# Kernel tuning notes

Hardware: AMD Instinct MI355X
Metric: run time of the kernel (lower is better)

Reference implementation:

```python
import jax, jax.numpy as jnp
import numpy as np

NB = 4
QN = -(2 ** (NB - 1))   # -8
QP = 2 ** (NB - 1) - 1  # 7
EPS = 1e-5


def _grad_scale(x, g):
    # forward: x, backward: grad * g (LSQ gradient scaling)
    return x * g + jax.lax.stop_gradient(x - x * g)


def _round_pass(x):
    # round with straight-through estimator
    return x + jax.lax.stop_gradient(jnp.round(x) - x)


def _lsq(v, alpha, qn, qp):
    # LSQ fake quantize-dequantize with learnable step size alpha
    g = 1.0 / np.sqrt(v.size * qp)
    a = _grad_scale(alpha, g)
    return _round_pass(jnp.clip(v / a, qn, qp)) * a


def _bn(x, g, b, m, v):
    # eval-mode BatchNorm2d over channel dim of NCHW
    s = (g * jax.lax.rsqrt(v + EPS))[None, :, None, None]
    return (x - m[None, :, None, None]) * s + b[None, :, None, None]


def _conv(x, w, stride, pad, groups):
    return jax.lax.conv_general_dilated(
        x, w, (stride, stride), pad,
        dimension_numbers=('NCHW', 'OIHW', 'NCHW'),
        feature_group_count=groups)


def setup_inputs() -> dict:
    key = jax.random.key(0)
    ks = jax.random.split(key, 4)
    inp, oup, hid = 96, 96, 576
    B, H, W = 32, 28, 28
    d = {}
    d['x'] = jax.random.normal(ks[0], (B, inp, H, W), jnp.float32)
    d['w1'] = jax.random.normal(ks[1], (hid, inp, 1, 1), jnp.float32) * 0.1
    d['w2'] = jax.random.normal(ks[2], (hid, 1, 3, 3), jnp.float32) * 0.1
    d['w3'] = jax.random.normal(ks[3], (oup, hid, 1, 1), jnp.float32) * 0.1
    for i, c in zip((1, 2, 3), (hid, hid, oup)):
        d[f'aw{i}'] = jnp.full((1,), 0.05, jnp.float32)  # weight step size
        d[f'ax{i}'] = jnp.full((1,), 0.5, jnp.float32)   # activation step size
        d[f'g{i}'] = jnp.ones((c,), jnp.float32)
        d[f'b{i}'] = jnp.zeros((c,), jnp.float32)
        d[f'm{i}'] = jnp.zeros((c,), jnp.float32)
        d[f'v{i}'] = jnp.ones((c,), jnp.float32)
    return d


def reference(x, w1, w2, w3, aw1, ax1, g1, b1, m1, v1,
              aw2, ax2, g2, b2, m2, v2, aw3, ax3, g3, b3, m3, v3):
    hid = w1.shape[0]
    # 1x1 expand conv (LSQ on activation and weight)
    h = _conv(_lsq(x, ax1, QN, QP), _lsq(w1, aw1, QN, QP), 1, [(0, 0), (0, 0)], 1)
    h = jnp.clip(_bn(h, g1, b1, m1, v1), 0.0, 6.0)
    # 3x3 depthwise conv, stride 1
    h = _conv(_lsq(h, ax2, QN, QP), _lsq(w2, aw2, QN, QP), 1, [(1, 1), (1, 1)], hid)
    h = jnp.clip(_bn(h, g2, b2, m2, v2), 0.0, 6.0)
    # 1x1 project conv
    h = _conv(_lsq(h, ax3, QN, QP), _lsq(w3, aw3, QN, QP), 1, [(0, 0), (0, 0)], 1)
    h = _bn(h, g3, b3, m3, v3)
    # identity residual (stride==1 and inp==oup)
    return x + h
```

## Files before the change

### kernel.cpp

```cpp
#include <hip/hip_runtime.h>

#define EPSF 1e-5f

typedef int      int4v   __attribute__((ext_vector_type(4)));
typedef int      int2v   __attribute__((ext_vector_type(2)));
typedef float    float4v __attribute__((ext_vector_type(4)));
typedef _Float16 half8   __attribute__((ext_vector_type(8)));
typedef _Float16 half4   __attribute__((ext_vector_type(4)));

#define QH1H_OFF 0
#define QH2T_OFF 28901376
#define W1P_OFF  43352064
#define W3P_OFF  (W1P_OFF + 55296)
#define W2H_OFF  (W3P_OFF + 55296)
#define S1B1_OFF (W2H_OFF + 10368)
#define S2B2_OFF (S1B1_OFF + 4608)
#define S3B3_OFF (S2B2_OFF + 4608)

__device__ __forceinline__ float lsq_q(float v, float a) {
    float t = v / a;
    t = fminf(fmaxf(t, -8.0f), 7.0f);
    return rintf(t);
}

__device__ __forceinline__ long q8pack_w(const float* s, float a) {
    unsigned long long v = 0;
    #pragma unroll
    for (int j = 0; j < 8; ++j) {
        int q = (int)lsq_q(s[j], a);
        v |= (unsigned long long)(q & 255) << (8 * j);
    }
    return (long)v;
}

__global__ __launch_bounds__(256)
void prep_w(const float* __restrict__ w1, const float* __restrict__ w2,
            const float* __restrict__ w3,
            const float* aw1, const float* ax1, const float* ax2,
            const float* aw2, const float* ax3, const float* aw3,
            const float* __restrict__ g1, const float* __restrict__ b1,
            const float* __restrict__ m1, const float* __restrict__ v1,
            const float* __restrict__ g2, const float* __restrict__ b2,
            const float* __restrict__ m2, const float* __restrict__ v2,
            const float* __restrict__ g3, const float* __restrict__ b3,
            const float* __restrict__ m3, const float* __restrict__ v3,
            long* __restrict__ w1p, long* __restrict__ w3p,
            _Float16* __restrict__ w2h,
            float* __restrict__ s1b1, float* __restrict__ s2b2,
            float* __restrict__ s3b3) {
    int id = blockIdx.x * 256 + threadIdx.x;
    if (id < 6912) {
        int l = id & 63, t = id >> 6;
        int kc = t % 3, ct = t / 3;
        int co = ct * 16 + (l & 15);
        int ci0 = kc * 32 + (l >> 4) * 8;
        w1p[id] = q8pack_w(w1 + co * 96 + ci0, aw1[0]);
    } else if (id < 13824) {
        int i = id - 6912;
        int l = i & 63, t = i >> 6;
        int kc = t % 18, ct = t / 18;
        int co = ct * 16 + (l & 15);
        int ci0 = kc * 32 + (l >> 4) * 8;
        w3p[i] = q8pack_w(w3 + co * 576 + ci0, aw3[0]);
    } else if (id < 19008) {
        int i = id - 13824;
        int c = i % 576, tap = i / 576;
        w2h[i] = (_Float16)lsq_q(w2[c * 9 + tap], aw2[0]);
    } else if (id < 19584) {
        int c = id - 19008;
        float s = g1[c] / sqrtf(v1[c] + EPSF);
        float A = aw1[0] * ax1[0];
        float inv = 1.0f / ax2[0];
        s1b1[c] = A * s * inv;
        s1b1[576 + c] = (b1[c] - m1[c] * s) * inv;
    } else if (id < 20160) {
        int c = id - 19584;
        float s = g2[c] / sqrtf(v2[c] + EPSF);
        float A = ax2[0] * aw2[0];
        float inv = 1.0f / ax3[0];
        s2b2[c] = A * s * inv;
        s2b2[576 + c] = (b2[c] - m2[c] * s) * inv;
    } else if (id < 20256) {
        int c = id - 20160;
        float s = g3[c] / sqrtf(v3[c] + EPSF);
        float A = ax3[0] * aw3[0];
        s3b3[c] = A * s;
        s3b3[96 + c] = b3[c] - m3[c] * s;
    }
}

__global__ __launch_bounds__(256)
void conv1_mfma(const float* __restrict__ x, const long* __restrict__ w1p,
                const float* ax1, const float* __restrict__ s1b1,
                _Float16* __restrict__ qh1h) {
    const int tid = threadIdx.x;
    const int w = tid >> 6, l = tid & 63;
    const int quad = l >> 4, c16 = l & 15;
    const int n0 = blockIdx.x * 64, cs = blockIdx.y;
    const int n = n0 + w * 16 + c16;
    const int bi = n / 784, p = n - bi * 784;
    const float inv1 = 1.0f / ax1[0];

    long bfr[3];
    #pragma unroll
    for (int kc = 0; kc < 3; ++kc) {
        const float* xs = x + (bi * 96 + kc * 32 + quad * 8) * 784 + p;
        unsigned long long v = 0;
        #pragma unroll
        for (int j = 0; j < 8; ++j) {
            float t = xs[j * 784] * inv1;
            t = fminf(fmaxf(t, -8.0f), 7.0f);
            int q = (int)rintf(t);
            v |= (unsigned long long)(q & 255) << (8 * j);
        }
        bfr[kc] = (long)v;
    }

    int4v acc[12];
    #pragma unroll
    for (int i = 0; i < 12; ++i) { acc[i][0] = 0; acc[i][1] = 0; acc[i][2] = 0; acc[i][3] = 0; }

    #pragma unroll
    for (int kc = 0; kc < 3; ++kc)
        #pragma unroll
        for (int ct = 0; ct < 12; ++ct)
            acc[ct] = __builtin_amdgcn_mfma_i32_16x16x32_i8(
                w1p[((cs * 12 + ct) * 3 + kc) * 64 + l], bfr[kc], acc[ct], 0, 0, 0);

    _Float16* orow = qh1h + n * 576;
    #pragma unroll
    for (int ct = 0; ct < 12; ++ct) {
        int co0 = cs * 192 + ct * 16 + quad * 4;
        float4v S = *(const float4v*)(s1b1 + co0);
        float4v B = *(const float4v*)(s1b1 + 576 + co0);
        half4 h;
        #pragma unroll
        for (int r = 0; r < 4; ++r) {
            float t = fmaf((float)acc[ct][r], S[r], B[r]);
            t = fminf(fmaxf(t, 0.0f), 7.0f);
            h[r] = (_Float16)rintf(t);
        }
        *(half4*)(orow + co0) = h;
    }
}

__global__ __launch_bounds__(256)
void dw_k(const _Float16* __restrict__ qh1h, const _Float16* __restrict__ w2h,
          const float* __restrict__ s2b2, signed char* __restrict__ qh2T) {
    int idx = blockIdx.x * 256 + threadIdx.x;
    int n = idx / 72, g = idx - (idx / 72) * 72;
    int c0 = g * 8;
    int p = n % 784;
    int hh = p / 28, ww = p - hh * 28;
    const _Float16* base = qh1h + n * 576 + c0;

    half8 acc;
    #pragma unroll
    for (int j = 0; j < 8; ++j) acc[j] = (_Float16)0.0f;

    #pragma unroll
    for (int t = 0; t < 9; ++t) {
        const int dh = t / 3 - 1, dc = t % 3 - 1;
        int ih = hh + dh, iw = ww + dc;
        if (ih >= 0 && ih < 28 && iw >= 0 && iw < 28) {
            half8 xv = *(const half8*)(base + (dh * 28 + dc) * 576);
            half8 wv = *(const half8*)(w2h + t * 576 + c0);
            acc += xv * wv;
        }
    }

    int pk0 = 0, pk1 = 0;
    #pragma unroll
    for (int j = 0; j < 8; ++j) {
        int c = c0 + j;
        float t = fmaf((float)acc[j], s2b2[c], s2b2[576 + c]);
        t = fminf(fmaxf(t, 0.0f), 7.0f);
        int q = (int)rintf(t);
        if (j < 4) pk0 |= q << (8 * j);
        else       pk1 |= q << (8 * (j - 4));
    }
    int2v pk; pk[0] = pk0; pk[1] = pk1;
    *(int2v*)(qh2T + n * 576 + c0) = pk;
}

__global__ __launch_bounds__(384)
void conv3_mfma(const signed char* __restrict__ qh2T, const long* __restrict__ w3p,
                const float* __restrict__ x, const float* __restrict__ s3b3,
                float* __restrict__ out) {
    const int tid = threadIdx.x;
    const int w = tid >> 6, l = tid & 63;
    const int quad = l >> 4, c16 = l & 15;
    const int n0 = blockIdx.x * 16;
    const int n_m = n0 + c16;

    int4v acc;
    acc[0] = 0; acc[1] = 0; acc[2] = 0; acc[3] = 0;

    const signed char* arow = qh2T + n_m * 576 + quad * 8;
    #pragma unroll 6
    for (int kc = 0; kc < 18; ++kc) {
        long a = *(const long*)(arow + kc * 32);
        long b = w3p[(w * 18 + kc) * 64 + l];
        acc = __builtin_amdgcn_mfma_i32_16x16x32_i8(a, b, acc, 0, 0, 0);
    }

    const int co = w * 16 + c16;
    const float S = s3b3[co], B = s3b3[96 + co];
    const int nb = n0 + quad * 4;
    const int bi = nb / 784, p0 = nb - bi * 784;
    const int off = (bi * 96 + co) * 784 + p0;
    float4v xr = *(const float4v*)(x + off);
    float4v o;
    #pragma unroll
    for (int r = 0; r < 4; ++r)
        o[r] = fmaf((float)acc[r], S, B) + xr[r];
    *(float4v*)(out + off) = o;
}

extern "C" void kernel_launch(void* const* d_in, const int* in_sizes, int n_in,
                              void* d_out, int out_size, void* d_ws, size_t ws_size,
                              hipStream_t stream) {
    const float* x   = (const float*)d_in[0];
    const float* w1  = (const float*)d_in[1];
    const float* w2  = (const float*)d_in[2];
    const float* w3  = (const float*)d_in[3];
    const float* aw1 = (const float*)d_in[4];
    const float* ax1 = (const float*)d_in[5];
    const float* g1  = (const float*)d_in[6];
    const float* b1  = (const float*)d_in[7];
    const float* m1  = (const float*)d_in[8];
    const float* v1  = (const float*)d_in[9];
    const float* aw2 = (const float*)d_in[10];
    const float* ax2 = (const float*)d_in[11];
    const float* g2  = (const float*)d_in[12];
    const float* b2  = (const float*)d_in[13];
    const float* m2  = (const float*)d_in[14];
    const float* v2  = (const float*)d_in[15];
    const float* aw3 = (const float*)d_in[16];
    const float* ax3 = (const float*)d_in[17];
    const float* g3  = (const float*)d_in[18];
    const float* b3  = (const float*)d_in[19];
    const float* m3  = (const float*)d_in[20];
    const float* v3  = (const float*)d_in[21];

    char* ws = (char*)d_ws;
    _Float16* qh1h = (_Float16*)(ws + QH1H_OFF);
    signed char* qh2T = (signed char*)(ws + QH2T_OFF);
    long* w1p = (long*)(ws + W1P_OFF);
    long* w3p = (long*)(ws + W3P_OFF);
    _Float16* w2h = (_Float16*)(ws + W2H_OFF);
    float* s1b1 = (float*)(ws + S1B1_OFF);
    float* s2b2 = (float*)(ws + S2B2_OFF);
    float* s3b3 = (float*)(ws + S3B3_OFF);

    float* out = (float*)d_out;

    prep_w<<<80, 256, 0, stream>>>(w1, w2, w3, aw1, ax1, ax2, aw2, ax3, aw3,
                                   g1, b1, m1, v1, g2, b2, m2, v2, g3, b3, m3, v3,
                                   w1p, w3p, w2h, s1b1, s2b2, s3b3);
    dim3 grid1(392, 3);
    conv1_mfma<<<grid1, 256, 0, stream>>>(x, w1p, ax1, s1b1, qh1h);
    dw_k<<<7056, 256, 0, stream>>>(qh1h, w2h, s2b2, qh2T);
    conv3_mfma<<<1568, 384, 0, stream>>>(qh2T, w3p, x, s3b3, out);
}
```

Baseline: 163.1 us.

## Fuse expand, depthwise and project convs into one kernel with LDS intermediates

Replaces the three separate kernels (1x1 expand MFMA, depthwise 3x3, 1x1 project MFMA) with a single kernel per (batch, 2-row strip) that keeps the quantized hidden activations in shared memory as int8. This removes the large fp16 and int8 intermediate round trips through global memory. The depthwise conv now uses integer multiply-accumulate on packed int8 values instead of fp16 vector math. The cost is recomputing a one-row halo of the expand conv per block, a large LDS footprint and low occupancy, and poorer MFMA reuse because each block reloads all the weights.

```diff
diff --git a/kernel.cpp b/kernel.cpp
--- a/kernel.cpp
+++ b/kernel.cpp
@@ -2,20 +2,15 @@
 
 #define EPSF 1e-5f
 
-typedef int      int4v   __attribute__((ext_vector_type(4)));
-typedef int      int2v   __attribute__((ext_vector_type(2)));
-typedef float    float4v __attribute__((ext_vector_type(4)));
-typedef _Float16 half8   __attribute__((ext_vector_type(8)));
-typedef _Float16 half4   __attribute__((ext_vector_type(4)));
-
-#define QH1H_OFF 0
-#define QH2T_OFF 28901376
-#define W1P_OFF  43352064
-#define W3P_OFF  (W1P_OFF + 55296)
-#define W2H_OFF  (W3P_OFF + 55296)
-#define S1B1_OFF (W2H_OFF + 10368)
-#define S2B2_OFF (S1B1_OFF + 4608)
-#define S3B3_OFF (S2B2_OFF + 4608)
+typedef int    int4v   __attribute__((ext_vector_type(4)));
+typedef float  float4v __attribute__((ext_vector_type(4)));
+
+#define W1P_OFF  0
+#define W3P_OFF  55296
+#define W2QI_OFF 110592
+#define S1B1_OFF 115776
+#define S2B2_OFF 120384
+#define S3B3_OFF 124992
 
 __device__ __forceinline__ float lsq_q(float v, float a) {
     float t = v / a;
@@ -45,7 +40,7 @@
             const float* __restrict__ g3, const float* __restrict__ b3,
             const float* __restrict__ m3, const float* __restrict__ v3,
             long* __restrict__ w1p, long* __restrict__ w3p,
-            _Float16* __restrict__ w2h,
+            signed char* __restrict__ w2qi,
             float* __restrict__ s1b1, float* __restrict__ s2b2,
             float* __restrict__ s3b3) {
     int id = blockIdx.x * 256 + threadIdx.x;
@@ -65,7 +60,7 @@
     } else if (id < 19008) {
         int i = id - 13824;
         int c = i % 576, tap = i / 576;
-        w2h[i] = (_Float16)lsq_q(w2[c * 9 + tap], aw2[0]);
+        w2qi[i] = (signed char)(int)lsq_q(w2[c * 9 + tap], aw2[0]);
     } else if (id < 19584) {
         int c = id - 19008;
         float s = g1[c] / sqrtf(v1[c] + EPSF);
@@ -89,132 +84,130 @@
     }
 }
 
-__global__ __launch_bounds__(256)
-void conv1_mfma(const float* __restrict__ x, const long* __restrict__ w1p,
-                const float* ax1, const float* __restrict__ s1b1,
-                _Float16* __restrict__ qh1h) {
+__global__ __launch_bounds__(448, 4)
+void fused_k(const float* __restrict__ x, const long* __restrict__ w1p,
+             const signed char* __restrict__ w2qi, const long* __restrict__ w3p,
+             const float* __restrict__ ax1,
+             const float* __restrict__ s1b1, const float* __restrict__ s2b2,
+             const float* __restrict__ s3b3, float* __restrict__ out) {
+    __shared__ __align__(16) signed char h[112 * 592];
     const int tid = threadIdx.x;
     const int w = tid >> 6, l = tid & 63;
     const int quad = l >> 4, c16 = l & 15;
-    const int n0 = blockIdx.x * 64, cs = blockIdx.y;
-    const int n = n0 + w * 16 + c16;
-    const int bi = n / 784, p = n - bi * 784;
-    const float inv1 = 1.0f / ax1[0];
-
-    long bfr[3];
+    const int b = blockIdx.x;
+    const int r0 = blockIdx.y * 2;
+
+    {
+        const int lp = w * 16 + c16;
+        int row = r0 - 1 + lp / 28;
+        row = min(max(row, 0), 27);
+        const int p = row * 28 + lp % 28;
+        const float inv1 = 1.0f / ax1[0];
+
+        long bfr[3];
+        #pragma unroll
+        for (int kc = 0; kc < 3; ++kc) {
+            const float* xs = x + (b * 96 + kc * 32 + quad * 8) * 784 + p;
+            unsigned long long v = 0;
+            #pragma unroll
+            for (int j = 0; j < 8; ++j) {
+                float t = xs[j * 784] * inv1;
+                t = fminf(fmaxf(t, -8.0f), 7.0f);
+                int q = (int)rintf(t);
+                v |= (unsigned long long)(q & 255) << (8 * j);
+            }
+            bfr[kc] = (long)v;
+        }
+        #pragma unroll 4
+        for (int ct = 0; ct < 36; ++ct) {
+            int4v acc; acc[0] = 0; acc[1] = 0; acc[2] = 0; acc[3] = 0;
+            #pragma unroll
+            for (int kc = 0; kc < 3; ++kc)
+                acc = __builtin_amdgcn_mfma_i32_16x16x32_i8(
+                    w1p[(ct * 3 + kc) * 64 + l], bfr[kc], acc, 0, 0, 0);
+            const int co0 = ct * 16 + quad * 4;
+            float4v S = *(const float4v*)(s1b1 + co0);
+            float4v B = *(const float4v*)(s1b1 + 576 + co0);
+            int pk = 0;
+            #pragma unroll
+            for (int r = 0; r < 4; ++r) {
+                float t = fmaf((float)acc[r], S[r], B[r]);
+                t = fminf(fmaxf(t, 0.0f), 7.0f);
+                pk |= ((int)rintf(t)) << (8 * r);
+            }
+            *(int*)(h + lp * 592 + co0) = pk;
+        }
+    }
+    __syncthreads();
+
+    int res0[9], res1[9];
     #pragma unroll
-    for (int kc = 0; kc < 3; ++kc) {
-        const float* xs = x + (bi * 96 + kc * 32 + quad * 8) * 784 + p;
-        unsigned long long v = 0;
+    for (int i = 0; i < 9; ++i) {
+        const int idx = tid + 448 * i;
+        const int pos = idx / 72, g = idx - (idx / 72) * 72;
+        const int row_in = pos / 28, col = pos - (pos / 28) * 28;
+        int acc[8] = {0, 0, 0, 0, 0, 0, 0, 0};
+        #pragma unroll
+        for (int dh = -1; dh <= 1; ++dh) {
+            if ((unsigned)(r0 + row_in + dh) >= 28u) continue;
+            #pragma unroll
+            for (int dc = -1; dc <= 1; ++dc) {
+                if ((unsigned)(col + dc) >= 28u) continue;
+                const int lp = (row_in + 1 + dh) * 28 + col + dc;
+                const int2 xv = *(const int2*)(h + lp * 592 + g * 8);
+                const int tap = (dh + 1) * 3 + dc + 1;
+                const int w0 = *(const int*)(w2qi + tap * 576 + g * 8);
+                const int w1v = *(const int*)(w2qi + tap * 576 + g * 8 + 4);
+                #pragma unroll
+                for (int j = 0; j < 4; ++j) {
+                    acc[j]     += ((xv.x >> (8 * j)) & 15) * ((w0  << (24 - 8 * j)) >> 24);
+                    acc[4 + j] += ((xv.y >> (8 * j)) & 15) * ((w1v << (24 - 8 * j)) >> 24);
+                }
+            }
+        }
+        int pk0 = 0, pk1 = 0;
         #pragma unroll
         for (int j = 0; j < 8; ++j) {
-            float t = xs[j * 784] * inv1;
-            t = fminf(fmaxf(t, -8.0f), 7.0f);
-            int q = (int)rintf(t);
-            v |= (unsigned long long)(q & 255) << (8 * j);
-        }
-        bfr[kc] = (long)v;
-    }
-
-    int4v acc[12];
+            const int c = g * 8 + j;
+            float t = fmaf((float)acc[j], s2b2[c], s2b2[576 + c]);
+            t = fminf(fmaxf(t, 0.0f), 7.0f);
+            const int q = (int)rintf(t);
+            if (j < 4) pk0 |= q << (8 * j); else pk1 |= q << (8 * (j - 4));
+        }
+        res0[i] = pk0; res1[i] = pk1;
+    }
+    __syncthreads();
     #pragma unroll
-    for (int i = 0; i < 12; ++i) { acc[i][0] = 0; acc[i][1] = 0; acc[i][2] = 0; acc[i][3] = 0; }
-
-    #pragma unroll
-    for (int kc = 0; kc < 3; ++kc)
-        #pragma unroll
-        for (int ct = 0; ct < 12; ++ct)
-            acc[ct] = __builtin_amdgcn_mfma_i32_16x16x32_i8(
-                w1p[((cs * 12 + ct) * 3 + kc) * 64 + l], bfr[kc], acc[ct], 0, 0, 0);
-
-    _Float16* orow = qh1h + n * 576;
-    #pragma unroll
-    for (int ct = 0; ct < 12; ++ct) {
-        int co0 = cs * 192 + ct * 16 + quad * 4;
-        float4v S = *(const float4v*)(s1b1 + co0);
-        float4v B = *(const float4v*)(s1b1 + 576 + co0);
-        half4 h;
-        #pragma unroll
-        for (int r = 0; r < 4; ++r) {
-            float t = fmaf((float)acc[ct][r], S[r], B[r]);
-            t = fminf(fmaxf(t, 0.0f), 7.0f);
-            h[r] = (_Float16)rintf(t);
-        }
-        *(half4*)(orow + co0) = h;
-    }
-}
-
-__global__ __launch_bounds__(256)
-void dw_k(const _Float16* __restrict__ qh1h, const _Float16* __restrict__ w2h,
-          const float* __restrict__ s2b2, signed char* __restrict__ qh2T) {
-    int idx = blockIdx.x * 256 + threadIdx.x;
-    int n = idx / 72, g = idx - (idx / 72) * 72;
-    int c0 = g * 8;
-    int p = n % 784;
-    int hh = p / 28, ww = p - hh * 28;
-    const _Float16* base = qh1h + n * 576 + c0;
-
-    half8 acc;
-    #pragma unroll
-    for (int j = 0; j < 8; ++j) acc[j] = (_Float16)0.0f;
-
-    #pragma unroll
-    for (int t = 0; t < 9; ++t) {
-        const int dh = t / 3 - 1, dc = t % 3 - 1;
-        int ih = hh + dh, iw = ww + dc;
-        if (ih >= 0 && ih < 28 && iw >= 0 && iw < 28) {
-            half8 xv = *(const half8*)(base + (dh * 28 + dc) * 576);
-            half8 wv = *(const half8*)(w2h + t * 576 + c0);
-            acc += xv * wv;
-        }
-    }
-
-    int pk0 = 0, pk1 = 0;
-    #pragma unroll
-    for (int j = 0; j < 8; ++j) {
-        int c = c0 + j;
-        float t = fmaf((float)acc[j], s2b2[c], s2b2[576 + c]);
-        t = fminf(fmaxf(t, 0.0f), 7.0f);
-        int q = (int)rintf(t);
-        if (j < 4) pk0 |= q << (8 * j);
-        else       pk1 |= q << (8 * (j - 4));
-    }
-    int2v pk; pk[0] = pk0; pk[1] = pk1;
-    *(int2v*)(qh2T + n * 576 + c0) = pk;
-}
-
-__global__ __launch_bounds__(384)
-void conv3_mfma(const signed char* __restrict__ qh2T, const long* __restrict__ w3p,
-                const float* __restrict__ x, const float* __restrict__ s3b3,
-                float* __restrict__ out) {
-    const int tid = threadIdx.x;
-    const int w = tid >> 6, l = tid & 63;
-    const int quad = l >> 4, c16 = l & 15;
-    const int n0 = blockIdx.x * 16;
-    const int n_m = n0 + c16;
-
-    int4v acc;
-    acc[0] = 0; acc[1] = 0; acc[2] = 0; acc[3] = 0;
-
-    const signed char* arow = qh2T + n_m * 576 + quad * 8;
-    #pragma unroll 6
-    for (int kc = 0; kc < 18; ++kc) {
-        long a = *(const long*)(arow + kc * 32);
-        long b = w3p[(w * 18 + kc) * 64 + l];
-        acc = __builtin_amdgcn_mfma_i32_16x16x32_i8(a, b, acc, 0, 0, 0);
-    }
-
-    const int co = w * 16 + c16;
-    const float S = s3b3[co], B = s3b3[96 + co];
-    const int nb = n0 + quad * 4;
-    const int bi = nb / 784, p0 = nb - bi * 784;
-    const int off = (bi * 96 + co) * 784 + p0;
-    float4v xr = *(const float4v*)(x + off);
-    float4v o;
-    #pragma unroll
-    for (int r = 0; r < 4; ++r)
-        o[r] = fmaf((float)acc[r], S, B) + xr[r];
-    *(float4v*)(out + off) = o;
+    for (int i = 0; i < 9; ++i) {
+        const int idx = tid + 448 * i;
+        const int pos = idx / 72, g = idx - (idx / 72) * 72;
+        int2 pk; pk.x = res0[i]; pk.y = res1[i];
+        *(int2*)(h + pos * 592 + g * 8) = pk;
+    }
+    __syncthreads();
+
+    for (int t = w; t < 24; t += 7) {
+        const int nt = t / 6, ct = t - (t / 6) * 6;
+        int4v acc; acc[0] = 0; acc[1] = 0; acc[2] = 0; acc[3] = 0;
+        const signed char* arow = h + (nt * 16 + c16) * 592 + quad * 8;
+        #pragma unroll 6
+        for (int kc = 0; kc < 18; ++kc)
+            acc = __builtin_amdgcn_mfma_i32_16x16x32_i8(
+                *(const long*)(arow + kc * 32),
+                w3p[(ct * 18 + kc) * 64 + l], acc, 0, 0, 0);
+        const int nloc = nt * 16 + quad * 4;
+        if (nloc < 56) {
+            const int co = ct * 16 + c16;
+            const float S = s3b3[co], Bv = s3b3[96 + co];
+            const int off = (b * 96 + co) * 784 + r0 * 28 + nloc;
+            const float4v xr = *(const float4v*)(x + off);
+            float4v o;
+            #pragma unroll
+            for (int r = 0; r < 4; ++r)
+                o[r] = fmaf((float)acc[r], S, Bv) + xr[r];
+            *(float4v*)(out + off) = o;
+        }
+    }
 }
 
 extern "C" void kernel_launch(void* const* d_in, const int* in_sizes, int n_in,
@@ -244,11 +237,9 @@
     const float* v3  = (const float*)d_in[21];
 
     char* ws = (char*)d_ws;
-    _Float16* qh1h = (_Float16*)(ws + QH1H_OFF);
-    signed char* qh2T = (signed char*)(ws + QH2T_OFF);
     long* w1p = (long*)(ws + W1P_OFF);
     long* w3p = (long*)(ws + W3P_OFF);
-    _Float16* w2h = (_Float16*)(ws + W2H_OFF);
+    signed char* w2qi = (signed char*)(ws + W2QI_OFF);
     float* s1b1 = (float*)(ws + S1B1_OFF);
     float* s2b2 = (float*)(ws + S2B2_OFF);
     float* s3b3 = (float*)(ws + S3B3_OFF);
@@ -257,9 +248,7 @@
 
     prep_w<<<80, 256, 0, stream>>>(w1, w2, w3, aw1, ax1, ax2, aw2, ax3, aw3,
                                    g1, b1, m1, v1, g2, b2, m2, v2, g3, b3, m3, v3,
-                                   w1p, w3p, w2h, s1b1, s2b2, s3b3);
-    dim3 grid1(392, 3);
-    conv1_mfma<<<grid1, 256, 0, stream>>>(x, w1p, ax1, s1b1, qh1h);
-    dw_k<<<7056, 256, 0, stream>>>(qh1h, w2h, s2b2, qh2T);
-    conv3_mfma<<<1568, 384, 0, stream>>>(qh2T, w3p, x, s3b3, out);
-}
+                                   w1p, w3p, w2qi, s1b1, s2b2, s3b3);
+    dim3 grid(32, 14);
+    fused_k<<<grid, 448, 0, stream>>>(x, w1p, w2qi, w3p, ax1, s1b1, s2b2, s3b3, out);
+}
```

Result: slower. 171.7 us (+5.3%).
